# Optimization experiments

Measured on AMD Instinct MI355X. Metric: run time of the kernel, lower is better.

## Reference

```python
import jax, jax.numpy as jnp
import numpy as np

B, T, C = 512, 256, 384   # batch, seq (== block_size), n_embd
HS, BS = 64, 256          # head_size, block_size


def setup_inputs() -> dict:
    key = jax.random.key(0)
    ks = jax.random.split(key, 6)
    s = 1.0 / np.sqrt(C)
    s2 = 1.0 / np.sqrt(HS)
    return {
        "x": jax.random.normal(ks[0], (B, T, C), jnp.float32),
        "W_q": jax.random.normal(ks[1], (C, HS), jnp.float32) * s,
        "W_k": jax.random.normal(ks[2], (C, HS), jnp.float32) * s,
        "W_v": jax.random.normal(ks[3], (C, HS), jnp.float32) * s,
        "W_ql": jax.random.normal(ks[4], (HS, BS), jnp.float32) * s2,
        "W_kl": jax.random.normal(ks[5], (HS, BS), jnp.float32) * s2,
    }


def reference(x, W_q, W_k, W_v, W_ql, W_kl):
    # One head of self-attention, additive (tanh) score variant, eval mode.
    # x: [B,T,C]
    q = jnp.einsum("btc,ch->bth", x, W_q)          # [B,T,HS]
    k = jnp.einsum("btc,ch->bth", x, W_k)          # [B,T,HS]
    q_w = jnp.einsum("bth,hs->bts", q, W_ql)       # [B,T,BS]
    k_w = jnp.einsum("bth,hs->bts", k, W_kl)       # [B,T,BS]
    # NOTE: elementwise add (both [B,T,BS]) as in the torch code, then tanh.
    wei = jnp.tanh(q_w + k_w)                      # [B,T,T] since T == BS
    Tn = x.shape[1]
    causal = jnp.tril(jnp.ones((Tn, Tn), dtype=bool))
    wei = jnp.where(causal, wei, -jnp.inf)
    wei = jax.nn.softmax(wei, axis=-1)
    v = jnp.einsum("btc,ch->bth", x, W_v)          # [B,T,HS]
    out = jnp.einsum("bts,bsh->bth", wei, v)       # [B,T,HS]
    return out
```

## Files before the change

kernel.cpp:

```cpp
#include <hip/hip_runtime.h>

#define BATCH 512
#define TT    256
#define CC    384
#define HH    64

typedef float  f32x4 __attribute__((ext_vector_type(4)));
typedef short  s16x8 __attribute__((ext_vector_type(8)));

#define XS_OFF   0
#define WS_OFF   32768
#define VB_OFF   114688
#define SCR_OFF  147456
#define LDS_TOTAL 155648

__device__ __forceinline__ unsigned short f2bf(float f) {
    union { float f; unsigned u; } c; c.f = f;
    unsigned u = c.u;
    u += 0x7fffu + ((u >> 16) & 1u);
    return (unsigned short)(u >> 16);
}

__device__ __forceinline__ void gld_lds16(const void* g, void* l) {
    __builtin_amdgcn_global_load_lds(
        (const __attribute__((address_space(1))) unsigned int*)(unsigned long long)g,
        (__attribute__((address_space(3))) unsigned int*)(unsigned int)(unsigned long long)l,
        16, 0, 0);
}

__global__ void prep_w(const float* __restrict__ Wq, const float* __restrict__ Wk,
                       const float* __restrict__ Wv, const float* __restrict__ Wql,
                       const float* __restrict__ Wkl, unsigned short* __restrict__ wsW) {
    int gid = blockIdx.x * 256 + threadIdx.x;
    int k, n; float val;
    if (gid < CC * 256) {
        k = gid >> 8; int s = gid & 255; n = s;
        float acc = 0.f;
        for (int h = 0; h < HH; ++h)
            acc += Wq[k * HH + h] * Wql[h * 256 + s] + Wk[k * HH + h] * Wkl[h * 256 + s];
        val = acc;
    } else {
        int g2 = gid - CC * 256;
        k = g2 >> 6; int h = g2 & 63; n = 256 + h;
        val = Wv[k * HH + h];
    }
    int kc = k >> 6, kk = (k >> 5) & 1, ct = n >> 4;
    int lane = ((k >> 3) & 3) * 16 + (n & 15);
    int j = k & 7;
    wsW[((((kc * 2 + kk) * 20 + ct) * 64) + lane) * 8 + j] = f2bf(val);
}

__global__ __launch_bounds__(512, 2) void head_main(const float* __restrict__ x,
                                                    const unsigned short* __restrict__ wsW,
                                                    float* __restrict__ out) {
    extern __shared__ char sm[];
    unsigned short* Xs  = (unsigned short*)(sm + XS_OFF);
    unsigned short* Wsh = (unsigned short*)(sm + WS_OFF);
    unsigned short* Vb  = (unsigned short*)(sm + VB_OFF);

    const int b    = blockIdx.x;
    const int t    = threadIdx.x;
    const int w    = (t >> 6) & 7;
    const int lane = t & 63;
    const int q    = lane >> 4;
    const int cidx = lane & 15;
    const int rt0  = w;
    const int rt1  = 15 - w;
    unsigned short* scr = (unsigned short*)(sm + SCR_OFF) + w * 512;

    const float* xb = x + (size_t)b * (TT * CC);

    f32x4 accS0[8], accS1[16], accV[2][4];
#pragma unroll
    for (int i = 0; i < 8; ++i)  accS0[i] = (f32x4){0.f,0.f,0.f,0.f};
#pragma unroll
    for (int i = 0; i < 16; ++i) accS1[i] = (f32x4){0.f,0.f,0.f,0.f};
#pragma unroll
    for (int i = 0; i < 2; ++i)
#pragma unroll
        for (int j = 0; j < 4; ++j) accV[i][j] = (f32x4){0.f,0.f,0.f,0.f};

    int xrow[4], xkoff[4];
#pragma unroll
    for (int i = 0; i < 4; ++i) {
        int g = t + i * 512;
        int kk = g >> 10, rt = (g >> 6) & 15, L = g & 63;
        xrow[i]  = rt * 16 + (L & 15);
        xkoff[i] = kk * 32 + ((L >> 4) & 3) * 8;
    }

    float4 xf[8];
#pragma unroll
    for (int i = 0; i < 4; ++i) {
        const float4* p = (const float4*)(xb + xrow[i] * CC + xkoff[i]);
        xf[2*i]   = p[0];
        xf[2*i+1] = p[1];
    }
#pragma unroll
    for (int i = 0; i < 5; ++i) {
        int g = t + i * 512;
        gld_lds16(wsW + g * 8, Wsh + g * 8);
    }

    for (int kc = 0; kc < 6; ++kc) {
#pragma unroll
        for (int i = 0; i < 4; ++i) {
            int g = t + i * 512;
            float4 f0 = xf[2*i], f1 = xf[2*i+1];
            s16x8 v;
            v[0] = (short)f2bf(f0.x); v[1] = (short)f2bf(f0.y);
            v[2] = (short)f2bf(f0.z); v[3] = (short)f2bf(f0.w);
            v[4] = (short)f2bf(f1.x); v[5] = (short)f2bf(f1.y);
            v[6] = (short)f2bf(f1.z); v[7] = (short)f2bf(f1.w);
            *(s16x8*)(Xs + g * 8) = v;
        }
        __syncthreads();

        if (kc < 5) {
            const int kn = kc + 1;
#pragma unroll
            for (int i = 0; i < 4; ++i) {
                const float4* p = (const float4*)(xb + xrow[i] * CC + kn * 64 + xkoff[i]);
                xf[2*i]   = p[0];
                xf[2*i+1] = p[1];
            }
            const unsigned short* wsrc = wsW + (size_t)kn * 20480;
            unsigned short*       wdst = Wsh + (kn & 1) * 20480;
#pragma unroll
            for (int i = 0; i < 5; ++i) {
                int g = t + i * 512;
                gld_lds16(wsrc + g * 8, wdst + g * 8);
            }
        }

        const unsigned short* Wb = Wsh + (kc & 1) * 20480;
#pragma unroll
        for (int kk = 0; kk < 2; ++kk) {
            s16x8 a0 = *(const s16x8*)(Xs + ((kk * 16 + rt0) * 64 + lane) * 8);
            s16x8 a1 = *(const s16x8*)(Xs + ((kk * 16 + rt1) * 64 + lane) * 8);
#pragma unroll
            for (int ct = 0; ct < 16; ++ct) {
                if (ct <= rt1) {
                    s16x8 bf = *(const s16x8*)(Wb + ((kk * 20 + ct) * 64 + lane) * 8);
                    accS1[ct] = __builtin_amdgcn_mfma_f32_16x16x32_bf16(a1, bf, accS1[ct], 0, 0, 0);
                    if (ct < 8 && ct <= rt0)
                        accS0[ct] = __builtin_amdgcn_mfma_f32_16x16x32_bf16(a0, bf, accS0[ct], 0, 0, 0);
                }
            }
#pragma unroll
            for (int v2 = 0; v2 < 4; ++v2) {
                s16x8 bf = *(const s16x8*)(Wb + ((kk * 20 + 16 + v2) * 64 + lane) * 8);
                accV[0][v2] = __builtin_amdgcn_mfma_f32_16x16x32_bf16(a0, bf, accV[0][v2], 0, 0, 0);
                accV[1][v2] = __builtin_amdgcn_mfma_f32_16x16x32_bf16(a1, bf, accV[1][v2], 0, 0, 0);
            }
        }
        __syncthreads();
    }

    float rs0[4] = {0.f,0.f,0.f,0.f}, rs1[4] = {0.f,0.f,0.f,0.f};
    s16x8 pf0[4], pf1[8];

#pragma unroll
    for (int ch = 0; ch < 8; ++ch) {
        if (ch <= (rt1 >> 1)) {
#pragma unroll
            for (int sub = 0; sub < 2; ++sub) {
                const int ct = 2 * ch + sub;
                const int gcol = ct * 16 + cidx;
                const int c = sub * 16 + cidx;
#pragma unroll
                for (int rg = 0; rg < 4; ++rg) {
                    const int grow = rt1 * 16 + q * 4 + rg;
                    float e = 0.f;
                    if (ct <= rt1 && gcol <= grow) {
                        float sv = accS1[2 * ch + sub][rg];
                        float ex = __expf(2.f * sv);
                        float th = 1.f - __fdividef(2.f, ex + 1.f);
                        e = __expf(th);
                    }
                    rs1[rg] += e;
                    scr[((c >> 3) * 16 + q * 4 + rg) * 8 + (c & 7)] = f2bf(e);
                }
            }
            pf1[ch] = *(const s16x8*)(scr + lane * 8);
        }
    }
#pragma unroll
    for (int ch = 0; ch < 4; ++ch) {
        if (ch <= (rt0 >> 1)) {
#pragma unroll
            for (int sub = 0; sub < 2; ++sub) {
                const int ct = 2 * ch + sub;
                const int gcol = ct * 16 + cidx;
                const int c = sub * 16 + cidx;
#pragma unroll
                for (int rg = 0; rg < 4; ++rg) {
                    const int grow = rt0 * 16 + q * 4 + rg;
                    float e = 0.f;
                    if (ct <= rt0 && gcol <= grow) {
                        float sv = accS0[2 * ch + sub][rg];
                        float ex = __expf(2.f * sv);
                        float th = 1.f - __fdividef(2.f, ex + 1.f);
                        e = __expf(th);
                    }
                    rs0[rg] += e;
                    scr[((c >> 3) * 16 + q * 4 + rg) * 8 + (c & 7)] = f2bf(e);
                }
            }
            pf0[ch] = *(const s16x8*)(scr + lane * 8);
        }
    }

#pragma unroll
    for (int ri = 0; ri < 2; ++ri) {
        const int rt = ri ? rt1 : rt0;
#pragma unroll
        for (int vct = 0; vct < 4; ++vct)
#pragma unroll
            for (int rg = 0; rg < 4; ++rg) {
                int srow = rt * 16 + q * 4 + rg;
                Vb[((vct * 8 + (srow >> 5)) * 64 + ((srow >> 3) & 3) * 16 + cidx) * 8 + (srow & 7)] =
                    f2bf(accV[ri][vct][rg]);
            }
    }

#pragma unroll
    for (int rg = 0; rg < 4; ++rg) {
        float v0 = rs0[rg], v1 = rs1[rg];
        v0 += __shfl_xor(v0, 1); v0 += __shfl_xor(v0, 2);
        v0 += __shfl_xor(v0, 4); v0 += __shfl_xor(v0, 8);
        v1 += __shfl_xor(v1, 1); v1 += __shfl_xor(v1, 2);
        v1 += __shfl_xor(v1, 4); v1 += __shfl_xor(v1, 8);
        rs0[rg] = v0; rs1[rg] = v1;
    }

    __syncthreads();

    f32x4 acc2[2][4];
#pragma unroll
    for (int i = 0; i < 2; ++i)
#pragma unroll
        for (int j = 0; j < 4; ++j) acc2[i][j] = (f32x4){0.f,0.f,0.f,0.f};

    const int nch0 = rt0 >> 1, nch1 = rt1 >> 1;
#pragma unroll
    for (int ch = 0; ch < 8; ++ch) {
        if (ch <= nch1) {
            s16x8 vb[4];
#pragma unroll
            for (int vct = 0; vct < 4; ++vct)
                vb[vct] = *(const s16x8*)(Vb + ((vct * 8 + ch) * 64 + lane) * 8);
#pragma unroll
            for (int vct = 0; vct < 4; ++vct)
                acc2[1][vct] = __builtin_amdgcn_mfma_f32_16x16x32_bf16(pf1[ch], vb[vct], acc2[1][vct], 0, 0, 0);
            if (ch < 4 && ch <= nch0) {
#pragma unroll
                for (int vct = 0; vct < 4; ++vct)
                    acc2[0][vct] = __builtin_amdgcn_mfma_f32_16x16x32_bf16(pf0[ch], vb[vct], acc2[0][vct], 0, 0, 0);
            }
        }
    }

    float* ob = out + (size_t)b * (TT * HH);
#pragma unroll
    for (int ri = 0; ri < 2; ++ri) {
        const int rt = ri ? rt1 : rt0;
#pragma unroll
        for (int rg = 0; rg < 4; ++rg) {
            int row = rt * 16 + q * 4 + rg;
            float inv = __fdividef(1.f, ri ? rs1[rg] : rs0[rg]);
#pragma unroll
            for (int vct = 0; vct < 4; ++vct)
                ob[row * HH + vct * 16 + cidx] = acc2[ri][vct][rg] * inv;
        }
    }
}

extern "C" void kernel_launch(void* const* d_in, const int* in_sizes, int n_in,
                              void* d_out, int out_size, void* d_ws, size_t ws_size,
                              hipStream_t stream) {
    const float* x   = (const float*)d_in[0];
    const float* Wq  = (const float*)d_in[1];
    const float* Wk  = (const float*)d_in[2];
    const float* Wv  = (const float*)d_in[3];
    const float* Wql = (const float*)d_in[4];
    const float* Wkl = (const float*)d_in[5];
    unsigned short* wsW = (unsigned short*)d_ws;
    float* out = (float*)d_out;

    prep_w<<<480, 256, 0, stream>>>(Wq, Wk, Wv, Wql, Wkl, wsW);

    hipFuncSetAttribute((const void*)head_main,
                        hipFuncAttributeMaxDynamicSharedMemorySize, LDS_TOTAL);
    head_main<<<BATCH, 512, LDS_TOTAL, stream>>>(x, wsW, out);
}
```

Before: 321.0 us.

## Drop LDS staging of x and weights; load MFMA fragments directly from global

Removes the cooperative LDS staging of x tiles and the weight buffer. Each wave now loads its own x rows and the pre-swizzled weight fragments straight from global/L2 into registers, and V is computed in a separate pass before the score pass. This eliminates the block-wide barriers in the K loop and shrinks LDS use. In exchange, x is read twice, weight loads are no longer shared across waves, and the causal work skip is coarsened into groups of four tiles. Scratch is enlarged so each wave writes all probability chunks before reading them back.

```diff
diff --git a/kernel.cpp b/kernel.cpp
--- a/kernel.cpp
+++ b/kernel.cpp
@@ -8,11 +8,9 @@
 typedef float  f32x4 __attribute__((ext_vector_type(4)));
 typedef short  s16x8 __attribute__((ext_vector_type(8)));
 
-#define XS_OFF   0
-#define WS_OFF   32768
-#define VB_OFF   114688
-#define SCR_OFF  147456
-#define LDS_TOTAL 155648
+#define VB_OFF    0
+#define SCR_OFF   32768
+#define LDS_TOTAL 131072
 
 __device__ __forceinline__ unsigned short f2bf(float f) {
     union { float f; unsigned u; } c; c.f = f;
@@ -21,11 +19,13 @@
     return (unsigned short)(u >> 16);
 }
 
-__device__ __forceinline__ void gld_lds16(const void* g, void* l) {
-    __builtin_amdgcn_global_load_lds(
-        (const __attribute__((address_space(1))) unsigned int*)(unsigned long long)g,
-        (__attribute__((address_space(3))) unsigned int*)(unsigned int)(unsigned long long)l,
-        16, 0, 0);
+__device__ __forceinline__ s16x8 cvt8(float4 f0, float4 f1) {
+    s16x8 v;
+    v[0] = (short)f2bf(f0.x); v[1] = (short)f2bf(f0.y);
+    v[2] = (short)f2bf(f0.z); v[3] = (short)f2bf(f0.w);
+    v[4] = (short)f2bf(f1.x); v[5] = (short)f2bf(f1.y);
+    v[6] = (short)f2bf(f1.z); v[7] = (short)f2bf(f1.w);
+    return v;
 }
 
 __global__ void prep_w(const float* __restrict__ Wq, const float* __restrict__ Wk,
@@ -44,21 +44,18 @@
         k = g2 >> 6; int h = g2 & 63; n = 256 + h;
         val = Wv[k * HH + h];
     }
-    int kc = k >> 6, kk = (k >> 5) & 1, ct = n >> 4;
+    int kk2 = k >> 5, ct = n >> 4;
     int lane = ((k >> 3) & 3) * 16 + (n & 15);
     int j = k & 7;
-    wsW[((((kc * 2 + kk) * 20 + ct) * 64) + lane) * 8 + j] = f2bf(val);
+    wsW[(((kk2 * 20 + ct) * 64) + lane) * 8 + j] = f2bf(val);
 }
 
 __global__ __launch_bounds__(512, 2) void head_main(const float* __restrict__ x,
                                                     const unsigned short* __restrict__ wsW,
                                                     float* __restrict__ out) {
     extern __shared__ char sm[];
-    unsigned short* Xs  = (unsigned short*)(sm + XS_OFF);
-    unsigned short* Wsh = (unsigned short*)(sm + WS_OFF);
     unsigned short* Vb  = (unsigned short*)(sm + VB_OFF);
 
-    const int b    = blockIdx.x;
     const int t    = threadIdx.x;
     const int w    = (t >> 6) & 7;
     const int lane = t & 63;
@@ -66,103 +63,119 @@
     const int cidx = lane & 15;
     const int rt0  = w;
     const int rt1  = 15 - w;
-    unsigned short* scr = (unsigned short*)(sm + SCR_OFF) + w * 512;
-
-    const float* xb = x + (size_t)b * (TT * CC);
-
-    f32x4 accS0[8], accS1[16], accV[2][4];
+    unsigned short* scr = (unsigned short*)(sm + SCR_OFF + w * 12288);
+
+    const float* xb  = x + (size_t)blockIdx.x * (TT * CC);
+    const float* xa0 = xb + (rt0 * 16 + cidx) * CC + q * 8;
+    const float* xa1 = xb + (rt1 * 16 + cidx) * CC + q * 8;
+
+    f32x4 accV[2][4];
+#pragma unroll
+    for (int i = 0; i < 2; ++i)
+#pragma unroll
+        for (int j = 0; j < 4; ++j) accV[i][j] = (f32x4){0.f,0.f,0.f,0.f};
+    {
+        float4 p00 = *(const float4*)(xa0),     p01 = *(const float4*)(xa0 + 4);
+        float4 p10 = *(const float4*)(xa1),     p11 = *(const float4*)(xa1 + 4);
+        for (int kk = 0; kk < 12; ++kk) {
+            s16x8 a0 = cvt8(p00, p01), a1 = cvt8(p10, p11);
+            if (kk < 11) {
+                const float* n0 = xa0 + (kk + 1) * 32;
+                const float* n1 = xa1 + (kk + 1) * 32;
+                p00 = *(const float4*)(n0); p01 = *(const float4*)(n0 + 4);
+                p10 = *(const float4*)(n1); p11 = *(const float4*)(n1 + 4);
+            }
+            const unsigned short* wb = wsW + (size_t)kk * 10240 + 16 * 512 + lane * 8;
+            s16x8 b0 = *(const s16x8*)(wb);
+            s16x8 b1 = *(const s16x8*)(wb + 512);
+            s16x8 b2 = *(const s16x8*)(wb + 1024);
+            s16x8 b3 = *(const s16x8*)(wb + 1536);
+            accV[0][0] = __builtin_amdgcn_mfma_f32_16x16x32_bf16(a0, b0, accV[0][0], 0, 0, 0);
+            accV[1][0] = __builtin_amdgcn_mfma_f32_16x16x32_bf16(a1, b0, accV[1][0], 0, 0, 0);
+            accV[0][1] = __builtin_amdgcn_mfma_f32_16x16x32_bf16(a0, b1, accV[0][1], 0, 0, 0);
+            accV[1][1] = __builtin_amdgcn_mfma_f32_16x16x32_bf16(a1, b1, accV[1][1], 0, 0, 0);
+            accV[0][2] = __builtin_amdgcn_mfma_f32_16x16x32_bf16(a0, b2, accV[0][2], 0, 0, 0);
+            accV[1][2] = __builtin_amdgcn_mfma_f32_16x16x32_bf16(a1, b2, accV[1][2], 0, 0, 0);
+            accV[0][3] = __builtin_amdgcn_mfma_f32_16x16x32_bf16(a0, b3, accV[0][3], 0, 0, 0);
+            accV[1][3] = __builtin_amdgcn_mfma_f32_16x16x32_bf16(a1, b3, accV[1][3], 0, 0, 0);
+        }
+    }
+#pragma unroll
+    for (int ri = 0; ri < 2; ++ri) {
+        const int rt = ri ? rt1 : rt0;
+#pragma unroll
+        for (int vct = 0; vct < 4; ++vct)
+#pragma unroll
+            for (int rg = 0; rg < 4; ++rg) {
+                int srow = rt * 16 + q * 4 + rg;
+                Vb[((vct * 8 + (srow >> 5)) * 64 + ((srow >> 3) & 3) * 16 + cidx) * 8 + (srow & 7)] =
+                    f2bf(accV[ri][vct][rg]);
+            }
+    }
+
+    f32x4 accS1[16], accS0[8];
+#pragma unroll
+    for (int i = 0; i < 16; ++i) accS1[i] = (f32x4){0.f,0.f,0.f,0.f};
 #pragma unroll
     for (int i = 0; i < 8; ++i)  accS0[i] = (f32x4){0.f,0.f,0.f,0.f};
-#pragma unroll
-    for (int i = 0; i < 16; ++i) accS1[i] = (f32x4){0.f,0.f,0.f,0.f};
-#pragma unroll
-    for (int i = 0; i < 2; ++i)
-#pragma unroll
-        for (int j = 0; j < 4; ++j) accV[i][j] = (f32x4){0.f,0.f,0.f,0.f};
-
-    int xrow[4], xkoff[4];
-#pragma unroll
-    for (int i = 0; i < 4; ++i) {
-        int g = t + i * 512;
-        int kk = g >> 10, rt = (g >> 6) & 15, L = g & 63;
-        xrow[i]  = rt * 16 + (L & 15);
-        xkoff[i] = kk * 32 + ((L >> 4) & 3) * 8;
-    }
-
-    float4 xf[8];
-#pragma unroll
-    for (int i = 0; i < 4; ++i) {
-        const float4* p = (const float4*)(xb + xrow[i] * CC + xkoff[i]);
-        xf[2*i]   = p[0];
-        xf[2*i+1] = p[1];
-    }
-#pragma unroll
-    for (int i = 0; i < 5; ++i) {
-        int g = t + i * 512;
-        gld_lds16(wsW + g * 8, Wsh + g * 8);
-    }
-
-    for (int kc = 0; kc < 6; ++kc) {
-#pragma unroll
-        for (int i = 0; i < 4; ++i) {
-            int g = t + i * 512;
-            float4 f0 = xf[2*i], f1 = xf[2*i+1];
-            s16x8 v;
-            v[0] = (short)f2bf(f0.x); v[1] = (short)f2bf(f0.y);
-            v[2] = (short)f2bf(f0.z); v[3] = (short)f2bf(f0.w);
-            v[4] = (short)f2bf(f1.x); v[5] = (short)f2bf(f1.y);
-            v[6] = (short)f2bf(f1.z); v[7] = (short)f2bf(f1.w);
-            *(s16x8*)(Xs + g * 8) = v;
-        }
-        __syncthreads();
-
-        if (kc < 5) {
-            const int kn = kc + 1;
+
+    const bool ng4   = (rt1 >= 12);
+    const bool g0two = (rt0 >= 4);
+    {
+        float4 p00 = *(const float4*)(xa0),     p01 = *(const float4*)(xa0 + 4);
+        float4 p10 = *(const float4*)(xa1),     p11 = *(const float4*)(xa1 + 4);
+        for (int kk = 0; kk < 12; ++kk) {
+            s16x8 a0 = cvt8(p00, p01), a1 = cvt8(p10, p11);
+            if (kk < 11) {
+                const float* n0 = xa0 + (kk + 1) * 32;
+                const float* n1 = xa1 + (kk + 1) * 32;
+                p00 = *(const float4*)(n0); p01 = *(const float4*)(n0 + 4);
+                p10 = *(const float4*)(n1); p11 = *(const float4*)(n1 + 4);
+            }
+            const unsigned short* wb = wsW + (size_t)kk * 10240 + lane * 8;
+            s16x8 bfA[4], bfB[4];
+#pragma unroll
+            for (int i = 0; i < 4; ++i) bfA[i] = *(const s16x8*)(wb + i * 512);
+#pragma unroll
+            for (int i = 0; i < 4; ++i) bfB[i] = *(const s16x8*)(wb + (4 + i) * 512);
 #pragma unroll
             for (int i = 0; i < 4; ++i) {
-                const float4* p = (const float4*)(xb + xrow[i] * CC + kn * 64 + xkoff[i]);
-                xf[2*i]   = p[0];
-                xf[2*i+1] = p[1];
-            }
-            const unsigned short* wsrc = wsW + (size_t)kn * 20480;
-            unsigned short*       wdst = Wsh + (kn & 1) * 20480;
-#pragma unroll
-            for (int i = 0; i < 5; ++i) {
-                int g = t + i * 512;
-                gld_lds16(wsrc + g * 8, wdst + g * 8);
-            }
-        }
-
-        const unsigned short* Wb = Wsh + (kc & 1) * 20480;
-#pragma unroll
-        for (int kk = 0; kk < 2; ++kk) {
-            s16x8 a0 = *(const s16x8*)(Xs + ((kk * 16 + rt0) * 64 + lane) * 8);
-            s16x8 a1 = *(const s16x8*)(Xs + ((kk * 16 + rt1) * 64 + lane) * 8);
-#pragma unroll
-            for (int ct = 0; ct < 16; ++ct) {
-                if (ct <= rt1) {
-                    s16x8 bf = *(const s16x8*)(Wb + ((kk * 20 + ct) * 64 + lane) * 8);
-                    accS1[ct] = __builtin_amdgcn_mfma_f32_16x16x32_bf16(a1, bf, accS1[ct], 0, 0, 0);
-                    if (ct < 8 && ct <= rt0)
-                        accS0[ct] = __builtin_amdgcn_mfma_f32_16x16x32_bf16(a0, bf, accS0[ct], 0, 0, 0);
-                }
-            }
-#pragma unroll
-            for (int v2 = 0; v2 < 4; ++v2) {
-                s16x8 bf = *(const s16x8*)(Wb + ((kk * 20 + 16 + v2) * 64 + lane) * 8);
-                accV[0][v2] = __builtin_amdgcn_mfma_f32_16x16x32_bf16(a0, bf, accV[0][v2], 0, 0, 0);
-                accV[1][v2] = __builtin_amdgcn_mfma_f32_16x16x32_bf16(a1, bf, accV[1][v2], 0, 0, 0);
-            }
-        }
-        __syncthreads();
+                accS1[i] = __builtin_amdgcn_mfma_f32_16x16x32_bf16(a1, bfA[i], accS1[i], 0, 0, 0);
+                accS0[i] = __builtin_amdgcn_mfma_f32_16x16x32_bf16(a0, bfA[i], accS0[i], 0, 0, 0);
+            }
+#pragma unroll
+            for (int i = 0; i < 4; ++i) bfA[i] = *(const s16x8*)(wb + (8 + i) * 512);
+#pragma unroll
+            for (int i = 0; i < 4; ++i)
+                accS1[4 + i] = __builtin_amdgcn_mfma_f32_16x16x32_bf16(a1, bfB[i], accS1[4 + i], 0, 0, 0);
+            if (g0two) {
+#pragma unroll
+                for (int i = 0; i < 4; ++i)
+                    accS0[4 + i] = __builtin_amdgcn_mfma_f32_16x16x32_bf16(a0, bfB[i], accS0[4 + i], 0, 0, 0);
+            }
+            if (ng4) {
+#pragma unroll
+                for (int i = 0; i < 4; ++i) bfB[i] = *(const s16x8*)(wb + (12 + i) * 512);
+            }
+#pragma unroll
+            for (int i = 0; i < 4; ++i)
+                accS1[8 + i] = __builtin_amdgcn_mfma_f32_16x16x32_bf16(a1, bfA[i], accS1[8 + i], 0, 0, 0);
+            if (ng4) {
+#pragma unroll
+                for (int i = 0; i < 4; ++i)
+                    accS1[12 + i] = __builtin_amdgcn_mfma_f32_16x16x32_bf16(a1, bfB[i], accS1[12 + i], 0, 0, 0);
+            }
+        }
     }
 
     float rs0[4] = {0.f,0.f,0.f,0.f}, rs1[4] = {0.f,0.f,0.f,0.f};
     s16x8 pf0[4], pf1[8];
+    const int nch1 = rt1 >> 1;
+    const int nch0 = rt0 >> 1;
 
 #pragma unroll
     for (int ch = 0; ch < 8; ++ch) {
-        if (ch <= (rt1 >> 1)) {
+        if (ch <= nch1) {
 #pragma unroll
             for (int sub = 0; sub < 2; ++sub) {
                 const int ct = 2 * ch + sub;
@@ -173,21 +186,24 @@
                     const int grow = rt1 * 16 + q * 4 + rg;
                     float e = 0.f;
                     if (ct <= rt1 && gcol <= grow) {
-                        float sv = accS1[2 * ch + sub][rg];
+                        float sv = accS1[ct][rg];
                         float ex = __expf(2.f * sv);
                         float th = 1.f - __fdividef(2.f, ex + 1.f);
                         e = __expf(th);
                     }
                     rs1[rg] += e;
-                    scr[((c >> 3) * 16 + q * 4 + rg) * 8 + (c & 7)] = f2bf(e);
+                    scr[ch * 512 + ((c >> 3) * 16 + q * 4 + rg) * 8 + (c & 7)] = f2bf(e);
                 }
             }
-            pf1[ch] = *(const s16x8*)(scr + lane * 8);
-        }
-    }
+        }
+    }
+#pragma unroll
+    for (int ch = 0; ch < 8; ++ch)
+        if (ch <= nch1) pf1[ch] = *(const s16x8*)(scr + ch * 512 + lane * 8);
+
 #pragma unroll
     for (int ch = 0; ch < 4; ++ch) {
-        if (ch <= (rt0 >> 1)) {
+        if (ch <= nch0) {
 #pragma unroll
             for (int sub = 0; sub < 2; ++sub) {
                 const int ct = 2 * ch + sub;
@@ -198,31 +214,20 @@
                     const int grow = rt0 * 16 + q * 4 + rg;
                     float e = 0.f;
                     if (ct <= rt0 && gcol <= grow) {
-                        float sv = accS0[2 * ch + sub][rg];
+                        float sv = accS0[ct][rg];
                         float ex = __expf(2.f * sv);
                         float th = 1.f - __fdividef(2.f, ex + 1.f);
                         e = __expf(th);
                     }
                     rs0[rg] += e;
-                    scr[((c >> 3) * 16 + q * 4 + rg) * 8 + (c & 7)] = f2bf(e);
+                    scr[4096 + ch * 512 + ((c >> 3) * 16 + q * 4 + rg) * 8 + (c & 7)] = f2bf(e);
                 }
             }
-            pf0[ch] = *(const s16x8*)(scr + lane * 8);
-        }
-    }
-
-#pragma unroll
-    for (int ri = 0; ri < 2; ++ri) {
-        const int rt = ri ? rt1 : rt0;
-#pragma unroll
-        for (int vct = 0; vct < 4; ++vct)
-#pragma unroll
-            for (int rg = 0; rg < 4; ++rg) {
-                int srow = rt * 16 + q * 4 + rg;
-                Vb[((vct * 8 + (srow >> 5)) * 64 + ((srow >> 3) & 3) * 16 + cidx) * 8 + (srow & 7)] =
-                    f2bf(accV[ri][vct][rg]);
-            }
-    }
+        }
+    }
+#pragma unroll
+    for (int ch = 0; ch < 4; ++ch)
+        if (ch <= nch0) pf0[ch] = *(const s16x8*)(scr + 4096 + ch * 512 + lane * 8);
 
 #pragma unroll
     for (int rg = 0; rg < 4; ++rg) {
@@ -242,7 +247,6 @@
 #pragma unroll
         for (int j = 0; j < 4; ++j) acc2[i][j] = (f32x4){0.f,0.f,0.f,0.f};
 
-    const int nch0 = rt0 >> 1, nch1 = rt1 >> 1;
 #pragma unroll
     for (int ch = 0; ch < 8; ++ch) {
         if (ch <= nch1) {
@@ -261,7 +265,7 @@
         }
     }
 
-    float* ob = out + (size_t)b * (TT * HH);
+    float* ob = out + (size_t)blockIdx.x * (TT * HH);
 #pragma unroll
     for (int ri = 0; ri < 2; ++ri) {
         const int rt = ri ? rt1 : rt0;
```

After: 361.4 us. 12.6% more time.
